# Performance work log

Measured on AMD Instinct MI355X. Metric: run time of the kernel, lower is better.

Reference implementation:

```python
import jax, jax.numpy as jnp
import numpy as np

D_MODEL = 1024
D_STATE = 16
B, L = 4, 2048


def _ln(x, g, b, eps=1e-5):
    mu = x.mean(-1, keepdims=True)
    var = ((x - mu) ** 2).mean(-1, keepdims=True)
    return (x - mu) * jax.lax.rsqrt(var + eps) * g + b


def _selective_ssm(x, dt_w, dt_b, Bp_w, Bp_b, Cp_w, Cp_b, A_log, D_p):
    # x: (B, L, D)
    delta = jax.nn.softplus(x @ dt_w + dt_b)          # (B, L, D)
    Bt = x @ Bp_w + Bp_b                               # (B, L, N)
    Ct = x @ Cp_w + Cp_b                               # (B, L, N)
    A = -jnp.exp(A_log)                                # (D, N)

    def step(h, inp):
        xt, dt, bt, ct = inp                            # (B,D),(B,D),(B,N),(B,N)
        dA = jnp.exp(dt[..., None] * A)                 # (B, D, N)
        dBx = dt[..., None] * bt[:, None, :] * xt[..., None]
        h = dA * h + dBx                                # (B, D, N)
        y = jnp.einsum('bdn,bn->bd', h, ct)
        return h, y

    xs = (jnp.swapaxes(x, 0, 1), jnp.swapaxes(delta, 0, 1),
          jnp.swapaxes(Bt, 0, 1), jnp.swapaxes(Ct, 0, 1))
    h0 = jnp.zeros((x.shape[0], D_MODEL, D_STATE), dtype=x.dtype)
    _, ys = jax.lax.scan(step, h0, xs)                  # (L, B, D)
    return jnp.swapaxes(ys, 0, 1) + D_p * x


def _forward(x, ln1_g, ln1_b, ln_g, ln_b, w1_w, w1_b, v1_w, v1_b, w2_w, w2_b,
             conv_w, dt_w, dt_b, Bp_w, Bp_b, Cp_w, Cp_b, A_log, D_p,
             ln2_g, ln2_b, ff1_w, ff1_b, ff2_w, ff2_b):
    res = x
    xn = _ln(x, ln1_g, ln1_b)
    # --- MambaLayer ---
    xm = _ln(xn, ln_g, ln_b)
    x1 = xm @ w1_w + w1_b                               # (B, L, D)
    x1t = jnp.swapaxes(x1, 1, 2)                        # (B, D, L)
    xc = jax.lax.conv_general_dilated(
        x1t, conv_w, window_strides=(1,), padding=[(1, 1)],
        feature_group_count=D_MODEL,
        dimension_numbers=('NCH', 'OIH', 'NCH'))
    xc = jax.nn.silu(jnp.swapaxes(xc, 1, 2))            # (B, L, D)
    y = _selective_ssm(xc, dt_w, dt_b, Bp_w, Bp_b, Cp_w, Cp_b, A_log, D_p)
    v = jax.nn.silu(xm @ v1_w + v1_b)
    mo = (y * v) @ w2_w + w2_b
    # --- residual + FFN ---
    x = mo + res
    res2 = x
    xn2 = _ln(x, ln2_g, ln2_b)
    h = jax.nn.gelu(xn2 @ ff1_w + ff1_b, approximate=False)
    return h @ ff2_w + ff2_b + res2


def setup_inputs() -> dict:
    key = jax.random.key(0)
    ks = jax.random.split(key, 16)
    s = 0.02
    d, n = D_MODEL, D_STATE
    inp = {
        'x': jax.random.normal(ks[0], (B, L, d), jnp.float32),
        'ln1_g': jnp.ones((d,), jnp.float32), 'ln1_b': jnp.zeros((d,), jnp.float32),
        'ln_g': jnp.ones((d,), jnp.float32), 'ln_b': jnp.zeros((d,), jnp.float32),
        'w1_w': jax.random.normal(ks[1], (d, d), jnp.float32) * s,
        'w1_b': jnp.zeros((d,), jnp.float32),
        'v1_w': jax.random.normal(ks[2], (d, d), jnp.float32) * s,
        'v1_b': jnp.zeros((d,), jnp.float32),
        'w2_w': jax.random.normal(ks[3], (d, d), jnp.float32) * s,
        'w2_b': jnp.zeros((d,), jnp.float32),
        'conv_w': jax.random.normal(ks[4], (d, 1, 3), jnp.float32) * s,
        'dt_w': jax.random.normal(ks[5], (d, d), jnp.float32) * s,
        'dt_b': jnp.zeros((d,), jnp.float32),
        'Bp_w': jax.random.normal(ks[6], (d, n), jnp.float32) * s,
        'Bp_b': jnp.zeros((n,), jnp.float32),
        'Cp_w': jax.random.normal(ks[7], (d, n), jnp.float32) * s,
        'Cp_b': jnp.zeros((n,), jnp.float32),
        'A_log': jnp.tile(jnp.log(jnp.arange(1, n + 1, dtype=jnp.float32)), (d, 1)),
        'D_p': jnp.ones((d,), jnp.float32),
        'ln2_g': jnp.ones((d,), jnp.float32), 'ln2_b': jnp.zeros((d,), jnp.float32),
        'ff1_w': jax.random.normal(ks[8], (d, 3 * d), jnp.float32) * s,
        'ff1_b': jnp.zeros((3 * d,), jnp.float32),
        'ff2_w': jax.random.normal(ks[9], (3 * d, d), jnp.float32) * s,
        'ff2_b': jnp.zeros((d,), jnp.float32),
    }
    return inp


def reference(x, ln1_g, ln1_b, ln_g, ln_b, w1_w, w1_b, v1_w, v1_b, w2_w, w2_b,
              conv_w, dt_w, dt_b, Bp_w, Bp_b, Cp_w, Cp_b, A_log, D_p,
              ln2_g, ln2_b, ff1_w, ff1_b, ff2_w, ff2_b):
    return _forward(x, ln1_g, ln1_b, ln_g, ln_b, w1_w, w1_b, v1_w, v1_b, w2_w,
                    w2_b, conv_w, dt_w, dt_b, Bp_w, Bp_b, Cp_w, Cp_b, A_log,
                    D_p, ln2_g, ln2_b, ff1_w, ff1_b, ff2_w, ff2_b)
```

## Files before the change

kernel.cpp:

```cpp
#include <hip/hip_runtime.h>

typedef unsigned short u16;
typedef __attribute__((ext_vector_type(8))) short short8;
typedef __attribute__((ext_vector_type(4))) float f32x4;
typedef __attribute__((ext_vector_type(4))) unsigned short u16x4;

#define SEQ 2048
#define DM 1024
#define NTOK 8192
#define CH 64
#define NCH 32

__device__ __forceinline__ float b2f(u16 u) {
  union { float f; unsigned int i; } x; x.i = ((unsigned int)u) << 16; return x.f;
}
__device__ __forceinline__ u16 f2b(float f) {
  union { float f; unsigned int i; } x; x.f = f;
  unsigned int i = x.i;
  unsigned int r = (i + 0x7FFFu + ((i >> 16) & 1u)) >> 16;
  return (u16)r;
}

__device__ __forceinline__ void gload16(const u16* g, u16* l) {
  __builtin_amdgcn_global_load_lds(
      (const __attribute__((address_space(1))) void*)g,
      (__attribute__((address_space(3))) void*)l, 16, 0, 0);
}

__device__ __forceinline__ float gelu_f(float v) {
  const float z = fabsf(v) * 0.70710678118f;
  const float t = __builtin_amdgcn_rcpf(1.f + 0.3275911f * z);
  float poly = ((((1.061405429f * t - 1.453152027f) * t + 1.421413741f) * t
                 - 0.284496736f) * t + 0.254829592f) * t;
  float e = 1.f - poly * __expf(-z * z);
  float erfv = (v < 0.f) ? -e : e;
  return 0.5f * v * (1.f + erfv);
}
__device__ __forceinline__ float silu_f(float v) {
  return v * __builtin_amdgcn_rcpf(1.f + __expf(-v));
}
__device__ __forceinline__ float softplus_f(float v) {
  return fmaxf(v, 0.f) + __logf(1.f + __expf(-fabsf(v)));
}

__global__ __launch_bounds__(256)
void wtrans(const float* __restrict__ in, u16* __restrict__ out,
            int K, int N, int rowOff, int ldOut)
{
  __shared__ float tile[32][33];
  const int n0 = blockIdx.x * 32;
  const int k0 = blockIdx.y * 32;
  const int tx = threadIdx.x, ty = threadIdx.y;
#pragma unroll
  for (int i = 0; i < 32; i += 8) {
    int k = k0 + ty + i, n = n0 + tx;
    tile[ty + i][tx] = (k < K && n < N) ? in[(long)k * N + n] : 0.f;
  }
  __syncthreads();
#pragma unroll
  for (int i = 0; i < 32; i += 8) {
    int n = n0 + ty + i, k = k0 + tx;
    if (n < N && k < K) out[(long)(rowOff + n) * ldOut + k] = f2b(tile[tx][ty + i]);
  }
}

__global__ __launch_bounds__(256)
void wtrans4(const float* __restrict__ s0, const float* __restrict__ s1,
             const float* __restrict__ s2, const float* __restrict__ s3,
             u16* __restrict__ d0, u16* __restrict__ d1,
             u16* __restrict__ d2, u16* __restrict__ d3)
{
  __shared__ float tile[32][33];
  const float* in; u16* out;
  switch (blockIdx.z) {
    case 0: in = s0; out = d0; break;
    case 1: in = s1; out = d1; break;
    case 2: in = s2; out = d2; break;
    default: in = s3; out = d3; break;
  }
  const int n0 = blockIdx.x * 32;
  const int k0 = blockIdx.y * 32;
  const int tx = threadIdx.x, ty = threadIdx.y;
#pragma unroll
  for (int i = 0; i < 32; i += 8)
    tile[ty + i][tx] = in[(long)(k0 + ty + i) * 1024 + n0 + tx];
  __syncthreads();
#pragma unroll
  for (int i = 0; i < 32; i += 8)
    out[(long)(n0 + ty + i) * 1024 + k0 + tx] = f2b(tile[tx][ty + i]);
}

__global__ __launch_bounds__(256)
void small_trans(const float* __restrict__ Bp, const float* __restrict__ Cp,
                 u16* __restrict__ wcatT)
{
  int t = blockIdx.x * 256 + threadIdx.x;
  int n = t >> 10, k = t & 1023;
  wcatT[(long)(1024 + n) * 1024 + k] = f2b(Bp[(long)k * 16 + n]);
  wcatT[(long)(1040 + n) * 1024 + k] = f2b(Cp[(long)k * 16 + n]);
#pragma unroll
  for (int i = 0; i < 6; ++i)
    wcatT[(long)1056 * 1024 + i * 16384 + t] = 0;
}

__device__ __forceinline__ void blockReduce2(float& a, float& b, float* s)
{
#pragma unroll
  for (int off = 32; off > 0; off >>= 1) {
    a += __shfl_xor(a, off);
    b += __shfl_xor(b, off);
  }
  const int lane = threadIdx.x & 63, wid = threadIdx.x >> 6;
  __syncthreads();
  if (lane == 0) { s[wid] = a; s[4 + wid] = b; }
  __syncthreads();
  a = s[0] + s[1] + s[2] + s[3];
  b = s[4] + s[5] + s[6] + s[7];
}

__global__ __launch_bounds__(256)
void ln_ln_kernel(const float* __restrict__ x, const float* __restrict__ g1,
                  const float* __restrict__ b1, const float* __restrict__ g2,
                  const float* __restrict__ b2, u16* __restrict__ out)
{
  __shared__ float sred[8];
  const long row = blockIdx.x;
  const int t = threadIdx.x;
  const float4 xv = ((const float4*)(x + row * DM))[t];
  float s = xv.x + xv.y + xv.z + xv.w;
  float sq = xv.x * xv.x + xv.y * xv.y + xv.z * xv.z + xv.w * xv.w;
  blockReduce2(s, sq, sred);
  const float mu = s * (1.f / DM);
  const float rs = rsqrtf(sq * (1.f / DM) - mu * mu + 1e-5f);
  const float4 g1v = ((const float4*)g1)[t];
  const float4 b1v = ((const float4*)b1)[t];
  float xn[4];
  xn[0] = (xv.x - mu) * rs * g1v.x + b1v.x;
  xn[1] = (xv.y - mu) * rs * g1v.y + b1v.y;
  xn[2] = (xv.z - mu) * rs * g1v.z + b1v.z;
  xn[3] = (xv.w - mu) * rs * g1v.w + b1v.w;
  float s2 = xn[0] + xn[1] + xn[2] + xn[3];
  float sq2 = xn[0] * xn[0] + xn[1] * xn[1] + xn[2] * xn[2] + xn[3] * xn[3];
  blockReduce2(s2, sq2, sred);
  const float mu2 = s2 * (1.f / DM);
  const float rs2 = rsqrtf(sq2 * (1.f / DM) - mu2 * mu2 + 1e-5f);
  const float4 g2v = ((const float4*)g2)[t];
  const float4 b2v = ((const float4*)b2)[t];
  u16x4 o;
  o[0] = f2b((xn[0] - mu2) * rs2 * g2v.x + b2v.x);
  o[1] = f2b((xn[1] - mu2) * rs2 * g2v.y + b2v.y);
  o[2] = f2b((xn[2] - mu2) * rs2 * g2v.z + b2v.z);
  o[3] = f2b((xn[3] - mu2) * rs2 * g2v.w + b2v.w);
  *(u16x4*)(out + row * DM + t * 4) = o;
}

__global__ __launch_bounds__(256)
void ln_kernel(const float* __restrict__ x, const float* __restrict__ g,
               const float* __restrict__ b, u16* __restrict__ out)
{
  __shared__ float sred[8];
  const long row = blockIdx.x;
  const int t = threadIdx.x;
  const float4 xv = ((const float4*)(x + row * DM))[t];
  float s = xv.x + xv.y + xv.z + xv.w;
  float sq = xv.x * xv.x + xv.y * xv.y + xv.z * xv.z + xv.w * xv.w;
  blockReduce2(s, sq, sred);
  const float mu = s * (1.f / DM);
  const float rs = rsqrtf(sq * (1.f / DM) - mu * mu + 1e-5f);
  const float4 gv = ((const float4*)g)[t];
  const float4 bv = ((const float4*)b)[t];
  u16x4 o;
  o[0] = f2b((xv.x - mu) * rs * gv.x + bv.x);
  o[1] = f2b((xv.y - mu) * rs * gv.y + bv.y);
  o[2] = f2b((xv.z - mu) * rs * gv.z + bv.z);
  o[3] = f2b((xv.w - mu) * rs * gv.w + bv.w);
  *(u16x4*)(out + row * DM + t * 4) = o;
}

__global__ __launch_bounds__(256)
void conv_silu_kernel(const u16* __restrict__ x1, const float* __restrict__ w,
                      u16* __restrict__ xc)
{
  const long i8 = (long)blockIdx.x * 256 + threadIdx.x;
  const long base = i8 * 8;
  const int d0 = (int)(base & (DM - 1));
  const long m = base >> 10;
  const int l = (int)(m & (SEQ - 1));
  const short8 cv = *(const short8*)(x1 + base);
  short8 lv = {}, rv = {};
  if (l > 0) lv = *(const short8*)(x1 + base - DM);
  if (l < SEQ - 1) rv = *(const short8*)(x1 + base + DM);
  short8 o;
#pragma unroll
  for (int j = 0; j < 8; ++j) {
    const int d = d0 + j;
    const float a = b2f((u16)lv[j]) * w[d * 3 + 0] + b2f((u16)cv[j]) * w[d * 3 + 1]
                  + b2f((u16)rv[j]) * w[d * 3 + 2];
    o[j] = (short)f2b(silu_f(a));
  }
  *(short8*)(xc + base) = o;
}

template <int MODE, int BN>
__global__ __launch_bounds__(256)
void gemm_bt(const u16* __restrict__ A, const u16* __restrict__ BT,
             const float* __restrict__ bias, const float* __restrict__ bias2,
             const float* __restrict__ bias3, const float* __restrict__ resid,
             void* __restrict__ outp, void* __restrict__ outp2,
             int K, int ldOut, int nbx)
{
  constexpr int NF = BN / 32;
  constexpr int BSZ = BN * 32;
  __shared__ u16 lds_a[2][4096];
  __shared__ u16 lds_b[2][BSZ];
  const int t = threadIdx.x;
  const int lane = t & 63;
  const int wid = t >> 6;
  const int wr = wid >> 1, wc = wid & 1;

  int bid = blockIdx.x;
  const int qch = gridDim.x >> 3;
  bid = (bid & 7) * qch + (bid >> 3);
  const long brow = (long)(bid / nbx) * 128;
  const long bcol = (long)(bid % nbx) * BN;

  f32x4 acc[4][NF] = {};

  const int srow = t >> 2;
  const int sslot = (t & 3) ^ ((t >> 3) & 3);
  const u16* aPtr = A + (brow + srow) * (long)K + sslot * 8;
  const u16* bPtr = BT + (bcol + srow) * (long)K + sslot * 8;
  u16* la = &lds_a[0][t * 8];
  u16* lb = &lds_b[0][t * 8];
  const long rowStep = 64L * K;
  const int nk = K >> 5;

  const int rslot = (lane >> 4) ^ ((lane >> 1) & 3);
  const int koff = rslot * 8;
  const int arow = wr * 64 + (lane & 15);
  const int brw = (BN == 128 ? wc * 64 : wc * 32) + (lane & 15);

#define STAGE(kt, buf)                                                  \
  {                                                                     \
    const int k0_ = (kt) << 5;                                          \
    gload16(aPtr + k0_, la + (buf) * 4096);                             \
    gload16(aPtr + rowStep + k0_, la + (buf) * 4096 + 2048);            \
    gload16(bPtr + k0_, lb + (buf) * BSZ);                              \
    if constexpr (BN == 128)                                            \
      gload16(bPtr + rowStep + k0_, lb + (buf) * BSZ + 2048);           \
  }

  STAGE(0, 0);
  __syncthreads();
  int cur = 0;
  for (int kt = 0; kt < nk; ++kt) {
    if (kt + 1 < nk) STAGE(kt + 1, cur ^ 1);
    short8 af[4], bfr[NF];
#pragma unroll
    for (int m = 0; m < 4; ++m)
      af[m] = *(const short8*)&lds_a[cur][(arow + m * 16) * 32 + koff];
#pragma unroll
    for (int n = 0; n < NF; ++n)
      bfr[n] = *(const short8*)&lds_b[cur][(brw + n * 16) * 32 + koff];
#pragma unroll
    for (int m = 0; m < 4; ++m)
#pragma unroll
      for (int n = 0; n < NF; ++n)
        acc[m][n] = __builtin_amdgcn_mfma_f32_16x16x32_bf16(af[m], bfr[n], acc[m][n], 0, 0, 0);
    __syncthreads();
    cur ^= 1;
  }
#undef STAGE

  const int cc = lane & 15;
  const int r0 = (lane >> 4) * 4;
#pragma unroll
  for (int m = 0; m < 4; ++m) {
#pragma unroll
    for (int n = 0; n < NF; ++n) {
      const long col = bcol + (BN == 128 ? wc * 64 : wc * 32) + n * 16 + cc;
#pragma unroll
      for (int r = 0; r < 4; ++r) {
        const long row = brow + wr * 64 + m * 16 + r0 + r;
        float val = acc[m][n][r];
        if constexpr (MODE == 4) {
          if (col < 1024) {
            ((float*)outp)[row * 1152 + col] = softplus_f(val + bias[col]);
          } else if (col < 1040) {
            ((float*)outp)[row * 1152 + col] = val + bias2[col - 1024];
          } else if (col < 1056) {
            ((float*)outp)[row * 1152 + col] = val + bias3[col - 1040];
          }
        } else if constexpr (MODE == 5) {
          if (col < 1024) {
            val += bias[col];
            ((u16*)outp)[row * 1024 + col] = f2b(val);
          } else {
            ((u16*)outp2)[row * 1024 + col - 1024] = f2b(silu_f(val + bias2[col - 1024]));
          }
        } else {
          val += bias[col];
          if constexpr (MODE == 2) val = gelu_f(val);
          if constexpr (MODE == 3) {
            ((float*)outp)[row * ldOut + col] = val + resid[row * ldOut + col];
          } else {
            ((u16*)outp)[row * ldOut + col] = f2b(val);
          }
        }
      }
    }
  }
}

__global__ __launch_bounds__(256)
void scan_pass1(const u16* __restrict__ xc, const float* __restrict__ dtbc,
                const float* __restrict__ A_log, const float* __restrict__ D_p,
                float* __restrict__ hloc, float* __restrict__ sdt,
                u16* __restrict__ ylb, u16* __restrict__ cdb)
{
  const int bx = blockIdx.x;
  const int b = bx >> 9;
  const int ch = (bx >> 4) & 31;
  const int dBase = (bx & 15) * 64;
  const int t = threadIdx.x;
  const int dl = t >> 2;
  const int q = t & 3;
  const int d = dBase + dl;

  __shared__ float s_bc[32][32];
  __shared__ float s_dt[32][64];
  __shared__ u16 s_x[32][64];
  __shared__ u16 s_yl[32][64];
  __shared__ u16 s_cd[32][64];

  float Areg[4];
#pragma unroll
  for (int j = 0; j < 4; ++j) Areg[j] = -__expf(A_log[d * 16 + q * 4 + j]);
  const float Dp = D_p[d];
  float h[4] = {0.f, 0.f, 0.f, 0.f};
  float sAcc = 0.f;
  const long mBase = (long)b * SEQ + ch * CH;

  for (int c0 = 0; c0 < CH; c0 += 32) {
#pragma unroll
    for (int i = 0; i < 4; ++i) {
      int idx = i * 256 + t;
      int s = idx >> 5, j = idx & 31;
      s_bc[s][j] = dtbc[(mBase + c0 + s) * 1152 + 1024 + j];
    }
#pragma unroll
    for (int i = 0; i < 8; ++i) {
      int idx = i * 256 + t;
      int s = idx >> 6, j = idx & 63;
      long m = mBase + c0 + s;
      s_dt[s][j] = dtbc[m * 1152 + dBase + j];
      s_x[s][j] = xc[m * DM + dBase + j];
    }
    __syncthreads();
#pragma unroll 4
    for (int s = 0; s < 32; ++s) {
      const float dt = s_dt[s][dl];
      const float xt = b2f(s_x[s][dl]);
      const float p = dt * xt;
      sAcc += dt;
      float y = 0.f;
#pragma unroll
      for (int j = 0; j < 4; ++j) {
        h[j] = __expf(dt * Areg[j]) * h[j] + p * s_bc[s][q * 4 + j];
        y = fmaf(h[j], s_bc[s][16 + q * 4 + j], y);
      }
      y += __shfl_xor(y, 1);
      y += __shfl_xor(y, 2);
      if (q == 0) s_yl[s][dl] = f2b(y + Dp * xt);
      if (q == 1) s_cd[s][dl] = f2b(sAcc);
    }
    __syncthreads();
#pragma unroll
    for (int i = 0; i < 8; ++i) {
      int idx = i * 256 + t;
      int s = idx >> 6, j = idx & 63;
      long m = mBase + c0 + s;
      ylb[m * DM + dBase + j] = s_yl[s][j];
      cdb[m * DM + dBase + j] = s_cd[s][j];
    }
    __syncthreads();
  }
  const long base = (((long)b * NCH + ch) * 1024 + d) * 16 + q * 4;
  float4 hv; hv.x = h[0]; hv.y = h[1]; hv.z = h[2]; hv.w = h[3];
  *(float4*)&hloc[base] = hv;
  if (q == 0) sdt[((long)b * NCH + ch) * 1024 + d] = sAcc;
}

__global__ __launch_bounds__(256)
void scan_pass2(const float* __restrict__ A_log, const float* __restrict__ sdt,
                const float* __restrict__ hloc, float* __restrict__ hin)
{
  const int tid = blockIdx.x * 256 + threadIdx.x;
  const int b = tid >> 14;
  const int dn = tid & 16383;
  const int d = dn >> 4;
  const float A = -__expf(A_log[dn]);
  float h = 0.f;
  for (int c = 0; c < NCH; ++c) {
    const long idx = (((long)b * NCH + c) << 14) + dn;
    hin[idx] = h;
    h = __expf(A * sdt[((long)b * NCH + c) * 1024 + d]) * h + hloc[idx];
  }
}

__global__ __launch_bounds__(256)
void scan_fix(const float* __restrict__ dtbc, const u16* __restrict__ ylb,
              const u16* __restrict__ cdb, const u16* __restrict__ vg,
              const float* __restrict__ A_log, const float* __restrict__ hin,
              u16* __restrict__ yv)
{
  const int bx = blockIdx.x;
  const int b = bx >> 9;
  const int ch = (bx >> 4) & 31;
  const int dBase = (bx & 15) * 64;
  const int t = threadIdx.x;
  const int dl = t >> 2;
  const int q = t & 3;
  const int d = dBase + dl;

  __shared__ float s_c[32][16];
  __shared__ u16 s_cd[32][64];
  __shared__ u16 s_yl[32][64];
  __shared__ u16 s_v[32][64];
  __shared__ u16 s_o[32][64];

  float Areg[4];
#pragma unroll
  for (int j = 0; j < 4; ++j) Areg[j] = -__expf(A_log[d * 16 + q * 4 + j]);
  const float4 hv4 = *(const float4*)&hin[(((long)b * NCH + ch) * 1024 + d) * 16 + q * 4];
  const float hv[4] = {hv4.x, hv4.y, hv4.z, hv4.w};

  const long mBase = (long)b * SEQ + ch * CH;

  for (int c0 = 0; c0 < CH; c0 += 32) {
#pragma unroll
    for (int i = 0; i < 2; ++i) {
      int idx = i * 256 + t;
      int s = idx >> 4, j = idx & 15;
      s_c[s][j] = dtbc[(mBase + c0 + s) * 1152 + 1040 + j];
    }
#pragma unroll
    for (int i = 0; i < 8; ++i) {
      int idx = i * 256 + t;
      int s = idx >> 6, j = idx & 63;
      long m = mBase + c0 + s;
      s_cd[s][j] = cdb[m * DM + dBase + j];
      s_yl[s][j] = ylb[m * DM + dBase + j];
      s_v[s][j] = vg[m * DM + dBase + j];
    }
    __syncthreads();
#pragma unroll 4
    for (int s = 0; s < 32; ++s) {
      const float cd = b2f(s_cd[s][dl]);
      float corr = 0.f;
#pragma unroll
      for (int j = 0; j < 4; ++j)
        corr = fmaf(s_c[s][q * 4 + j] * hv[j], __expf(Areg[j] * cd), corr);
      corr += __shfl_xor(corr, 1);
      corr += __shfl_xor(corr, 2);
      if (q == 0)
        s_o[s][dl] = f2b((b2f(s_yl[s][dl]) + corr) * b2f(s_v[s][dl]));
    }
    __syncthreads();
#pragma unroll
    for (int i = 0; i < 8; ++i) {
      int idx = i * 256 + t;
      int s = idx >> 6, j = idx & 63;
      yv[(mBase + c0 + s) * DM + dBase + j] = s_o[s][j];
    }
    __syncthreads();
  }
}

extern "C" void kernel_launch(void* const* d_in, const int* in_sizes, int n_in,
                              void* d_out, int out_size, void* d_ws, size_t ws_size,
                              hipStream_t stream)
{
  (void)in_sizes; (void)n_in; (void)out_size; (void)ws_size;
  const float* x      = (const float*)d_in[0];
  const float* ln1_g  = (const float*)d_in[1];
  const float* ln1_b  = (const float*)d_in[2];
  const float* ln_g   = (const float*)d_in[3];
  const float* ln_b   = (const float*)d_in[4];
  const float* w1_w   = (const float*)d_in[5];
  const float* w1_b   = (const float*)d_in[6];
  const float* v1_w   = (const float*)d_in[7];
  const float* v1_b   = (const float*)d_in[8];
  const float* w2_w   = (const float*)d_in[9];
  const float* w2_b   = (const float*)d_in[10];
  const float* conv_w = (const float*)d_in[11];
  const float* dt_w   = (const float*)d_in[12];
  const float* dt_b   = (const float*)d_in[13];
  const float* Bp_w   = (const float*)d_in[14];
  const float* Bp_b   = (const float*)d_in[15];
  const float* Cp_w   = (const float*)d_in[16];
  const float* Cp_b   = (const float*)d_in[17];
  const float* A_log  = (const float*)d_in[18];
  const float* D_p    = (const float*)d_in[19];
  const float* ln2_g  = (const float*)d_in[20];
  const float* ln2_b  = (const float*)d_in[21];
  const float* ff1_w  = (const float*)d_in[22];
  const float* ff1_b  = (const float*)d_in[23];
  const float* ff2_w  = (const float*)d_in[24];
  const float* ff2_b  = (const float*)d_in[25];

  char* ws = (char*)d_ws;
  size_t cur = 0;
  auto alloc = [&](size_t bytes) -> void* {
    void* p = ws + cur;
    cur = (cur + bytes + 255) & ~(size_t)255;
    return p;
  };

  u16* wv1T  = (u16*)alloc((size_t)2048 * 1024 * 2);
  u16* w2T   = (u16*)alloc((size_t)1024 * 1024 * 2);
  u16* wcatT = (u16*)alloc((size_t)1152 * 1024 * 2);
  u16* ff1T  = (u16*)alloc((size_t)3072 * 1024 * 2);
  u16* ff2T  = (u16*)alloc((size_t)1024 * 3072 * 2);
  u16* xm    = (u16*)alloc((size_t)NTOK * DM * 2);
  u16* x1b   = (u16*)alloc((size_t)NTOK * DM * 2);
  u16* vb    = (u16*)alloc((size_t)NTOK * DM * 2);
  u16* xcb   = (u16*)alloc((size_t)NTOK * DM * 2);
  float* dtbc = (float*)alloc((size_t)NTOK * 1152 * 4);
  float* x2  = (float*)alloc((size_t)NTOK * DM * 4);
  float* hloc = (float*)alloc((size_t)4 * NCH * 1024 * 16 * 4);
  float* hin  = (float*)alloc((size_t)4 * NCH * 1024 * 16 * 4);
  float* sdtb = (float*)alloc((size_t)4 * NCH * 1024 * 4);
  u16* yvb  = xm;
  u16* xn2  = x1b;
  u16* ylb  = x1b;
  u16* cdb  = (u16*)x2;
  u16* hb   = xcb;

  const dim3 tb32(32, 8);
  wtrans4<<<dim3(32, 32, 4), tb32, 0, stream>>>(w1_w, v1_w, w2_w, dt_w,
                                                wv1T, wv1T + (size_t)1024 * 1024,
                                                w2T, wcatT);
  small_trans<<<64, 256, 0, stream>>>(Bp_w, Cp_w, wcatT);
  wtrans<<<dim3(96, 32), tb32, 0, stream>>>(ff1_w, ff1T, 1024, 3072, 0, 1024);
  wtrans<<<dim3(32, 96), tb32, 0, stream>>>(ff2_w, ff2T, 3072, 1024, 0, 3072);

  ln_ln_kernel<<<NTOK, 256, 0, stream>>>(x, ln1_g, ln1_b, ln_g, ln_b, xm);

  gemm_bt<5, 128><<<1024, 256, 0, stream>>>(xm, wv1T, w1_b, v1_b, nullptr, nullptr,
                                            x1b, vb, 1024, 1024, 16);

  conv_silu_kernel<<<(NTOK * DM) / (256 * 8), 256, 0, stream>>>(x1b, conv_w, xcb);

  gemm_bt<4, 64><<<1152, 256, 0, stream>>>(xcb, wcatT, dt_b, Bp_b, Cp_b, nullptr,
                                           dtbc, nullptr, 1024, 1152, 18);

  scan_pass1<<<2048, 256, 0, stream>>>(xcb, dtbc, A_log, D_p, hloc, sdtb, ylb, cdb);
  scan_pass2<<<256, 256, 0, stream>>>(A_log, sdtb, hloc, hin);
  scan_fix<<<2048, 256, 0, stream>>>(dtbc, ylb, cdb, vb, A_log, hin, yvb);

  gemm_bt<3, 64><<<1024, 256, 0, stream>>>(yvb, w2T, w2_b, nullptr, nullptr, x,
                                           x2, nullptr, 1024, 1024, 16);

  ln_kernel<<<NTOK, 256, 0, stream>>>(x2, ln2_g, ln2_b, xn2);

  gemm_bt<2, 128><<<1536, 256, 0, stream>>>(xn2, ff1T, ff1_b, nullptr, nullptr, nullptr,
                                            hb, nullptr, 1024, 3072, 24);

  gemm_bt<3, 64><<<1024, 256, 0, stream>>>(hb, ff2T, ff2_b, nullptr, nullptr, x2,
                                           d_out, nullptr, 3072, 1024, 16);
}
```

Measured before the change: 438.8 us.

## Shrink intermediates to bf16, split dt/BC buffers, deepen K-stage in FF2 GEMM

The dt output of the projection GEMM is now stored as bf16 in its own compact buffer, and B/C go to a separate 32-wide float buffer. The grid drops from 1152 to 1088 blocks, which removes the padded columns. The post-mixer residual x2 is kept in bf16, read by a new bf16 LayerNorm, and added back as bf16 in the final GEMM. That final GEMM now uses 128-wide tiles and stages two K-subtiles per sync, halving barriers. The change is meant to cut global memory traffic and sync overhead, but it gives up precision in dt and the residual path, which could hurt accuracy.

```diff
diff --git a/kernel.cpp b/kernel.cpp
--- a/kernel.cpp
+++ b/kernel.cpp
@@ -155,25 +155,28 @@
 }
 
 __global__ __launch_bounds__(256)
-void ln_kernel(const float* __restrict__ x, const float* __restrict__ g,
-               const float* __restrict__ b, u16* __restrict__ out)
+void ln_bf_kernel(const u16* __restrict__ x, const float* __restrict__ g,
+                  const float* __restrict__ b, u16* __restrict__ out)
 {
   __shared__ float sred[8];
   const long row = blockIdx.x;
   const int t = threadIdx.x;
-  const float4 xv = ((const float4*)(x + row * DM))[t];
-  float s = xv.x + xv.y + xv.z + xv.w;
-  float sq = xv.x * xv.x + xv.y * xv.y + xv.z * xv.z + xv.w * xv.w;
+  const u16x4 xv4 = ((const u16x4*)(x + row * DM))[t];
+  float xv[4];
+#pragma unroll
+  for (int j = 0; j < 4; ++j) xv[j] = b2f(xv4[j]);
+  float s = xv[0] + xv[1] + xv[2] + xv[3];
+  float sq = xv[0] * xv[0] + xv[1] * xv[1] + xv[2] * xv[2] + xv[3] * xv[3];
   blockReduce2(s, sq, sred);
   const float mu = s * (1.f / DM);
   const float rs = rsqrtf(sq * (1.f / DM) - mu * mu + 1e-5f);
   const float4 gv = ((const float4*)g)[t];
   const float4 bv = ((const float4*)b)[t];
   u16x4 o;
-  o[0] = f2b((xv.x - mu) * rs * gv.x + bv.x);
-  o[1] = f2b((xv.y - mu) * rs * gv.y + bv.y);
-  o[2] = f2b((xv.z - mu) * rs * gv.z + bv.z);
-  o[3] = f2b((xv.w - mu) * rs * gv.w + bv.w);
+  o[0] = f2b((xv[0] - mu) * rs * gv.x + bv.x);
+  o[1] = f2b((xv[1] - mu) * rs * gv.y + bv.y);
+  o[2] = f2b((xv[2] - mu) * rs * gv.z + bv.z);
+  o[3] = f2b((xv[3] - mu) * rs * gv.w + bv.w);
   *(u16x4*)(out + row * DM + t * 4) = o;
 }
 
@@ -201,7 +204,7 @@
   *(short8*)(xc + base) = o;
 }
 
-template <int MODE, int BN>
+template <int MODE, int BN, int NU>
 __global__ __launch_bounds__(256)
 void gemm_bt(const u16* __restrict__ A, const u16* __restrict__ BT,
              const float* __restrict__ bias, const float* __restrict__ bias2,
@@ -210,8 +213,10 @@
              int K, int ldOut, int nbx)
 {
   constexpr int NF = BN / 32;
-  constexpr int BSZ = BN * 32;
-  __shared__ u16 lds_a[2][4096];
+  constexpr int ASZ = 4096 * NU;
+  constexpr int BSUB = BN * 32;
+  constexpr int BSZ = BSUB * NU;
+  __shared__ u16 lds_a[2][ASZ];
   __shared__ u16 lds_b[2][BSZ];
   const int t = threadIdx.x;
   const int lane = t & 63;
@@ -233,21 +238,24 @@
   u16* la = &lds_a[0][t * 8];
   u16* lb = &lds_b[0][t * 8];
   const long rowStep = 64L * K;
-  const int nk = K >> 5;
+  const int nk = K / (32 * NU);
 
   const int rslot = (lane >> 4) ^ ((lane >> 1) & 3);
   const int koff = rslot * 8;
   const int arow = wr * 64 + (lane & 15);
   const int brw = (BN == 128 ? wc * 64 : wc * 32) + (lane & 15);
 
-#define STAGE(kt, buf)                                                  \
-  {                                                                     \
-    const int k0_ = (kt) << 5;                                          \
-    gload16(aPtr + k0_, la + (buf) * 4096);                             \
-    gload16(aPtr + rowStep + k0_, la + (buf) * 4096 + 2048);            \
-    gload16(bPtr + k0_, lb + (buf) * BSZ);                              \
-    if constexpr (BN == 128)                                            \
-      gload16(bPtr + rowStep + k0_, lb + (buf) * BSZ + 2048);           \
+#define STAGE(kt, buf)                                                        \
+  {                                                                           \
+    _Pragma("unroll")                                                         \
+    for (int su_ = 0; su_ < NU; ++su_) {                                      \
+      const int k0_ = (((kt) * NU + su_) << 5);                               \
+      gload16(aPtr + k0_, la + (buf) * ASZ + su_ * 4096);                     \
+      gload16(aPtr + rowStep + k0_, la + (buf) * ASZ + su_ * 4096 + 2048);    \
+      gload16(bPtr + k0_, lb + (buf) * BSZ + su_ * BSUB);                     \
+      if constexpr (BN == 128)                                                \
+        gload16(bPtr + rowStep + k0_, lb + (buf) * BSZ + su_ * BSUB + 2048);  \
+    }                                                                         \
   }
 
   STAGE(0, 0);
@@ -255,18 +263,23 @@
   int cur = 0;
   for (int kt = 0; kt < nk; ++kt) {
     if (kt + 1 < nk) STAGE(kt + 1, cur ^ 1);
-    short8 af[4], bfr[NF];
-#pragma unroll
-    for (int m = 0; m < 4; ++m)
-      af[m] = *(const short8*)&lds_a[cur][(arow + m * 16) * 32 + koff];
-#pragma unroll
-    for (int n = 0; n < NF; ++n)
-      bfr[n] = *(const short8*)&lds_b[cur][(brw + n * 16) * 32 + koff];
-#pragma unroll
-    for (int m = 0; m < 4; ++m)
+#pragma unroll
+    for (int su = 0; su < NU; ++su) {
+      const u16* pa = &lds_a[cur][su * 4096];
+      const u16* pb = &lds_b[cur][su * BSUB];
+      short8 af[4], bfr[NF];
+#pragma unroll
+      for (int m = 0; m < 4; ++m)
+        af[m] = *(const short8*)&pa[(arow + m * 16) * 32 + koff];
 #pragma unroll
       for (int n = 0; n < NF; ++n)
-        acc[m][n] = __builtin_amdgcn_mfma_f32_16x16x32_bf16(af[m], bfr[n], acc[m][n], 0, 0, 0);
+        bfr[n] = *(const short8*)&pb[(brw + n * 16) * 32 + koff];
+#pragma unroll
+      for (int m = 0; m < 4; ++m)
+#pragma unroll
+        for (int n = 0; n < NF; ++n)
+          acc[m][n] = __builtin_amdgcn_mfma_f32_16x16x32_bf16(af[m], bfr[n], acc[m][n], 0, 0, 0);
+    }
     __syncthreads();
     cur ^= 1;
   }
@@ -285,11 +298,11 @@
         float val = acc[m][n][r];
         if constexpr (MODE == 4) {
           if (col < 1024) {
-            ((float*)outp)[row * 1152 + col] = softplus_f(val + bias[col]);
+            ((u16*)outp)[row * 1024 + col] = f2b(softplus_f(val + bias[col]));
           } else if (col < 1040) {
-            ((float*)outp)[row * 1152 + col] = val + bias2[col - 1024];
+            ((float*)outp2)[row * 32 + col - 1024] = val + bias2[col - 1024];
           } else if (col < 1056) {
-            ((float*)outp)[row * 1152 + col] = val + bias3[col - 1040];
+            ((float*)outp2)[row * 32 + col - 1024] = val + bias3[col - 1040];
           }
         } else if constexpr (MODE == 5) {
           if (col < 1024) {
@@ -298,14 +311,14 @@
           } else {
             ((u16*)outp2)[row * 1024 + col - 1024] = f2b(silu_f(val + bias2[col - 1024]));
           }
+        } else if constexpr (MODE == 6) {
+          val += bias[col];
+          ((u16*)outp)[row * ldOut + col] = f2b(val + resid[row * ldOut + col]);
+        } else if constexpr (MODE == 7) {
+          val += bias[col];
+          ((float*)outp)[row * ldOut + col] = val + b2f(((const u16*)resid)[row * ldOut + col]);
         } else {
-          val += bias[col];
-          if constexpr (MODE == 2) val = gelu_f(val);
-          if constexpr (MODE == 3) {
-            ((float*)outp)[row * ldOut + col] = val + resid[row * ldOut + col];
-          } else {
-            ((u16*)outp)[row * ldOut + col] = f2b(val);
-          }
+          ((u16*)outp)[row * ldOut + col] = f2b(gelu_f(val + bias[col]));
         }
       }
     }
@@ -313,10 +326,10 @@
 }
 
 __global__ __launch_bounds__(256)
-void scan_pass1(const u16* __restrict__ xc, const float* __restrict__ dtbc,
-                const float* __restrict__ A_log, const float* __restrict__ D_p,
-                float* __restrict__ hloc, float* __restrict__ sdt,
-                u16* __restrict__ ylb, u16* __restrict__ cdb)
+void scan_pass1(const u16* __restrict__ xc, const u16* __restrict__ dtb,
+                const float* __restrict__ bcb, const float* __restrict__ A_log,
+                const float* __restrict__ D_p, float* __restrict__ hloc,
+                float* __restrict__ sdt, u16* __restrict__ ylb, u16* __restrict__ cdb)
 {
   const int bx = blockIdx.x;
   const int b = bx >> 9;
@@ -328,7 +341,7 @@
   const int d = dBase + dl;
 
   __shared__ float s_bc[32][32];
-  __shared__ float s_dt[32][64];
+  __shared__ u16 s_dt[32][64];
   __shared__ u16 s_x[32][64];
   __shared__ u16 s_yl[32][64];
   __shared__ u16 s_cd[32][64];
@@ -346,20 +359,20 @@
     for (int i = 0; i < 4; ++i) {
       int idx = i * 256 + t;
       int s = idx >> 5, j = idx & 31;
-      s_bc[s][j] = dtbc[(mBase + c0 + s) * 1152 + 1024 + j];
+      s_bc[s][j] = bcb[(mBase + c0 + s) * 32 + j];
     }
 #pragma unroll
     for (int i = 0; i < 8; ++i) {
       int idx = i * 256 + t;
       int s = idx >> 6, j = idx & 63;
       long m = mBase + c0 + s;
-      s_dt[s][j] = dtbc[m * 1152 + dBase + j];
+      s_dt[s][j] = dtb[m * DM + dBase + j];
       s_x[s][j] = xc[m * DM + dBase + j];
     }
     __syncthreads();
 #pragma unroll 4
     for (int s = 0; s < 32; ++s) {
-      const float dt = s_dt[s][dl];
+      const float dt = b2f(s_dt[s][dl]);
       const float xt = b2f(s_x[s][dl]);
       const float p = dt * xt;
       sAcc += dt;
@@ -409,7 +422,7 @@
 }
 
 __global__ __launch_bounds__(256)
-void scan_fix(const float* __restrict__ dtbc, const u16* __restrict__ ylb,
+void scan_fix(const float* __restrict__ bcb, const u16* __restrict__ ylb,
               const u16* __restrict__ cdb, const u16* __restrict__ vg,
               const float* __restrict__ A_log, const float* __restrict__ hin,
               u16* __restrict__ yv)
@@ -442,7 +455,7 @@
     for (int i = 0; i < 2; ++i) {
       int idx = i * 256 + t;
       int s = idx >> 4, j = idx & 15;
-      s_c[s][j] = dtbc[(mBase + c0 + s) * 1152 + 1040 + j];
+      s_c[s][j] = bcb[(mBase + c0 + s) * 32 + 16 + j];
     }
 #pragma unroll
     for (int i = 0; i < 8; ++i) {
@@ -526,16 +539,17 @@
   u16* x1b   = (u16*)alloc((size_t)NTOK * DM * 2);
   u16* vb    = (u16*)alloc((size_t)NTOK * DM * 2);
   u16* xcb   = (u16*)alloc((size_t)NTOK * DM * 2);
-  float* dtbc = (float*)alloc((size_t)NTOK * 1152 * 4);
-  float* x2  = (float*)alloc((size_t)NTOK * DM * 4);
+  u16* dtb   = (u16*)alloc((size_t)NTOK * DM * 2);
+  float* bcb = (float*)alloc((size_t)NTOK * 32 * 4);
+  u16* x2u   = (u16*)alloc((size_t)NTOK * DM * 2);
   float* hloc = (float*)alloc((size_t)4 * NCH * 1024 * 16 * 4);
   float* hin  = (float*)alloc((size_t)4 * NCH * 1024 * 16 * 4);
   float* sdtb = (float*)alloc((size_t)4 * NCH * 1024 * 4);
   u16* yvb  = xm;
+  u16* ylb  = x1b;
   u16* xn2  = x1b;
-  u16* ylb  = x1b;
-  u16* cdb  = (u16*)x2;
-  u16* hb   = xcb;
+  u16* cdb  = x2u;
+  u16* hb   = vb;
 
   const dim3 tb32(32, 8);
   wtrans4<<<dim3(32, 32, 4), tb32, 0, stream>>>(w1_w, v1_w, w2_w, dt_w,
@@ -547,26 +561,27 @@
 
   ln_ln_kernel<<<NTOK, 256, 0, stream>>>(x, ln1_g, ln1_b, ln_g, ln_b, xm);
 
-  gemm_bt<5, 128><<<1024, 256, 0, stream>>>(xm, wv1T, w1_b, v1_b, nullptr, nullptr,
-                                            x1b, vb, 1024, 1024, 16);
+  gemm_bt<5, 128, 1><<<1024, 256, 0, stream>>>(xm, wv1T, w1_b, v1_b, nullptr, nullptr,
+                                               x1b, vb, 1024, 1024, 16);
 
   conv_silu_kernel<<<(NTOK * DM) / (256 * 8), 256, 0, stream>>>(x1b, conv_w, xcb);
 
-  gemm_bt<4, 64><<<1152, 256, 0, stream>>>(xcb, wcatT, dt_b, Bp_b, Cp_b, nullptr,
-                                           dtbc, nullptr, 1024, 1152, 18);
-
-  scan_pass1<<<2048, 256, 0, stream>>>(xcb, dtbc, A_log, D_p, hloc, sdtb, ylb, cdb);
+  gemm_bt<4, 64, 1><<<1088, 256, 0, stream>>>(xcb, wcatT, dt_b, Bp_b, Cp_b, nullptr,
+                                              dtb, bcb, 1024, 1024, 17);
+
+  scan_pass1<<<2048, 256, 0, stream>>>(xcb, dtb, bcb, A_log, D_p, hloc, sdtb, ylb, cdb);
   scan_pass2<<<256, 256, 0, stream>>>(A_log, sdtb, hloc, hin);
-  scan_fix<<<2048, 256, 0, stream>>>(dtbc, ylb, cdb, vb, A_log, hin, yvb);
-
-  gemm_bt<3, 64><<<1024, 256, 0, stream>>>(yvb, w2T, w2_b, nullptr, nullptr, x,
-                                           x2, nullptr, 1024, 1024, 16);
-
-  ln_kernel<<<NTOK, 256, 0, stream>>>(x2, ln2_g, ln2_b, xn2);
-
-  gemm_bt<2, 128><<<1536, 256, 0, stream>>>(xn2, ff1T, ff1_b, nullptr, nullptr, nullptr,
-                                            hb, nullptr, 1024, 3072, 24);
-
-  gemm_bt<3, 64><<<1024, 256, 0, stream>>>(hb, ff2T, ff2_b, nullptr, nullptr, x2,
-                                           d_out, nullptr, 3072, 1024, 16);
-}
+  scan_fix<<<2048, 256, 0, stream>>>(bcb, ylb, cdb, vb, A_log, hin, yvb);
+
+  gemm_bt<6, 64, 1><<<1024, 256, 0, stream>>>(yvb, w2T, w2_b, nullptr, nullptr, x,
+                                              x2u, nullptr, 1024, 1024, 16);
+
+  ln_bf_kernel<<<NTOK, 256, 0, stream>>>(x2u, ln2_g, ln2_b, xn2);
+
+  gemm_bt<2, 128, 1><<<1536, 256, 0, stream>>>(xn2, ff1T, ff1_b, nullptr, nullptr, nullptr,
+                                               hb, nullptr, 1024, 3072, 24);
+
+  gemm_bt<7, 128, 2><<<512, 256, 0, stream>>>(hb, ff2T, ff2_b, nullptr, nullptr,
+                                              (const float*)x2u, d_out, nullptr,
+                                              3072, 1024, 8);
+}
```

Result: faster. 419.7 us (-4.4%).
